# Kernel optimization log

Hardware: AMD Instinct MI355X
Metric: run time of the kernel (lower is better)

## Reference

```python
import jax, jax.numpy as jnp
import numpy as np

K_STEPS = 12      # number_of_prediction_steps
TEMP = 0.1        # temperature
EPS = 1e-12       # F.normalize eps


def setup_inputs() -> dict:
    key = jax.random.key(0)
    ks = jax.random.split(key, 8)
    B, T, W, D, C = 128, 512, 64, 128, 256
    g = lambda k, shape, s: (jax.random.normal(k, shape, jnp.float32) * s)
    return {
        "rr_windows": jax.random.normal(ks[0], (B, T, W), jnp.float32),
        # Encoder: Linear(window_size -> latent_dim)
        "We": g(ks[1], (W, D), 0.1), "be": jnp.zeros((D,), jnp.float32),
        # ARBlock: single-layer GRU(latent_dim -> context_dim)
        "Wi": g(ks[2], (D, 3 * C), 0.1), "Wh": g(ks[3], (C, 3 * C), 0.1),
        "bi": jnp.zeros((3 * C,), jnp.float32), "bh": jnp.zeros((3 * C,), jnp.float32),
        # Wk: K_STEPS Linears(context_dim -> latent_dim), stacked
        "Wk_w": g(ks[4], (K_STEPS, C, D), 0.1), "Wk_b": jnp.zeros((K_STEPS, D), jnp.float32),
    }


def _l2norm(x):
    n = jnp.linalg.norm(x, axis=-1, keepdims=True)
    return x / jnp.maximum(n, EPS)


def _gru(z_seq, Wi, Wh, bi, bh):
    # z_seq: [B, T, D] -> contexts [B, T, C]
    B = z_seq.shape[0]
    C = Wh.shape[0]
    x_proj = z_seq @ Wi + bi                       # [B, T, 3C] (precompute input gates)

    def step(h, x):
        hg = h @ Wh + bh
        xr, xz, xn = jnp.split(x, 3, axis=-1)
        hr, hz, hn = jnp.split(hg, 3, axis=-1)
        r = jax.nn.sigmoid(xr + hr)
        z = jax.nn.sigmoid(xz + hz)
        n = jnp.tanh(xn + r * hn)
        h_new = (1.0 - z) * n + z * h
        return h_new, h_new

    h0 = jnp.zeros((B, C), z_seq.dtype)
    _, hs = jax.lax.scan(step, h0, jnp.swapaxes(x_proj, 0, 1))  # [T, B, C]
    return jnp.swapaxes(hs, 0, 1)


def reference(rr_windows, We, be, Wi, Wh, bi, bh, Wk_w, Wk_b):
    B, T, W = rr_windows.shape
    # Encoder + normalize
    z_seq = _l2norm(rr_windows @ We + be)          # [B, T, D]
    # AR context
    c_seq = _gru(z_seq, Wi, Wh, bi, bh)            # [B, T, C]

    Tp = T - K_STEPS
    c_t = c_seq[:, :Tp, :]                         # [B, Tp, C]
    # all K predictions at once, then normalize
    pred = jnp.einsum('btc,kcd->kbtd', c_t, Wk_w) + Wk_b[:, None, None, :]
    pred = _l2norm(pred)                           # [K, B, Tp, D]
    # z_future[k, :, t] = z_seq[:, t + k + 1]
    zf = jnp.stack([jax.lax.dynamic_slice_in_dim(z_seq, k + 1, Tp, axis=1)
                    for k in range(K_STEPS)])      # [K, B, Tp, D]
    # logits[k, t, i, j] = pred[k, i, t] . z_future[k, j, t] / temp
    logits = jnp.einsum('kbtd,kctd->ktbc', pred, zf) / TEMP  # [K, Tp, B, B]

    lse = jax.nn.logsumexp(logits, axis=-1)        # [K, Tp, B]
    diag = jnp.einsum('ktbb->ktb', logits)
    avg_loss = jnp.mean(lse - diag)
    labels = jnp.arange(B)
    avg_accuracy = jnp.mean((jnp.argmax(logits, axis=-1) == labels).astype(jnp.float32)) * 100.0
    return avg_loss, avg_accuracy, z_seq, c_seq
```

## Files before the change

### kernel.cpp

```cpp
#include <hip/hip_runtime.h>
#include <math.h>

#define B_  128
#define T_  512
#define W_  64
#define D_  128
#define C_  256
#define K_  12
#define TP_ 500
#define N_SAMPLES 768000

typedef _Float16 half2v __attribute__((ext_vector_type(2)));
typedef _Float16 f16x8  __attribute__((ext_vector_type(8)));
typedef float    f32x4  __attribute__((ext_vector_type(4)));

__device__ __forceinline__ unsigned int pack2(float a, float b) {
  unsigned short ua = __builtin_bit_cast(unsigned short, (_Float16)a);
  unsigned short ub = __builtin_bit_cast(unsigned short, (_Float16)b);
  return (unsigned int)ua | ((unsigned int)ub << 16);
}

__global__ __launch_bounds__(128) void z_kernel(const float* __restrict__ rr,
                                                const float* __restrict__ We,
                                                const float* __restrict__ be,
                                                float* __restrict__ z_out,
                                                _Float16* __restrict__ z16) {
  int row = blockIdx.x;
  int d   = threadIdx.x;
  __shared__ float s_rr[64];
  __shared__ float s_w[2];
  if (d < 64) s_rr[d] = rr[row * 64 + d];
  __syncthreads();
  float acc = be[d];
#pragma unroll
  for (int w = 0; w < 64; ++w) acc = fmaf(s_rr[w], We[w * 128 + d], acc);
  float ss = acc * acc;
#pragma unroll
  for (int s = 1; s <= 32; s <<= 1) ss += __shfl_xor(ss, s);
  if ((d & 63) == 0) s_w[d >> 6] = ss;
  __syncthreads();
  float inv = 1.0f / fmaxf(sqrtf(s_w[0] + s_w[1]), 1e-12f);
  float zv = acc * inv;
  z_out[row * 128 + d] = zv;
  z16[(size_t)row * 128 + d] = (_Float16)zv;
}

__global__ __launch_bounds__(256) void wiT_kernel(const float* __restrict__ Wi,
                                                  _Float16* __restrict__ wiT) {
  int id = blockIdx.x * 256 + threadIdx.x;
  int k   = id / 768;
  int col = id % 768;
  wiT[(size_t)col * 128 + k] = (_Float16)Wi[id];
}

__global__ __launch_bounds__(256, 2) void xproj_mfma(const _Float16* __restrict__ z16,
                                                     const _Float16* __restrict__ wiT,
                                                     const float* __restrict__ bi,
                                                     _Float16* __restrict__ xp) {
  int rb  = blockIdx.x * 128;
  int cb  = blockIdx.y * 128;
  int tid  = threadIdx.x;
  int wv   = tid >> 6;
  int lane = tid & 63;
  int n15  = lane & 15;
  int q    = lane >> 4;

  __shared__ __align__(16) _Float16 sA[128 * 72];
  __shared__ __align__(16) _Float16 sB[128 * 72];

  f32x4 acc[2][8];
#pragma unroll
  for (int a = 0; a < 2; ++a)
#pragma unroll
    for (int m = 0; m < 8; ++m) acc[a][m] = (f32x4){0.f, 0.f, 0.f, 0.f};

#pragma unroll
  for (int p = 0; p < 2; ++p) {
#pragma unroll
    for (int it = 0; it < 4; ++it) {
      int id = tid + it * 256;
      int r  = id >> 3;
      int c8 = (id & 7) * 8;
      *(uint4*)(&sA[r * 72 + c8]) =
          *(const uint4*)(z16 + (size_t)(rb + r) * 128 + p * 64 + c8);
      *(uint4*)(&sB[r * 72 + c8]) =
          *(const uint4*)(wiT + (size_t)(cb + r) * 128 + p * 64 + c8);
    }
    __syncthreads();
#pragma unroll
    for (int ks = 0; ks < 2; ++ks) {
      f16x8 bf[2];
#pragma unroll
      for (int ntl = 0; ntl < 2; ++ntl)
        bf[ntl] = *(const f16x8*)(&sB[((wv * 2 + ntl) * 16 + n15) * 72 + ks * 32 + q * 8]);
#pragma unroll
      for (int mt = 0; mt < 8; ++mt) {
        f16x8 af = *(const f16x8*)(&sA[(mt * 16 + n15) * 72 + ks * 32 + q * 8]);
        acc[0][mt] = __builtin_amdgcn_mfma_f32_16x16x32_f16(af, bf[0], acc[0][mt], 0, 0, 0);
        acc[1][mt] = __builtin_amdgcn_mfma_f32_16x16x32_f16(af, bf[1], acc[1][mt], 0, 0, 0);
      }
    }
    __syncthreads();
  }

#pragma unroll
  for (int ntl = 0; ntl < 2; ++ntl) {
    int col = cb + (wv * 2 + ntl) * 16 + n15;
    float bb = bi[col];
#pragma unroll
    for (int mt = 0; mt < 8; ++mt) {
#pragma unroll
      for (int r = 0; r < 4; ++r) {
        int row = rb + mt * 16 + q * 4 + r;
        xp[(size_t)row * 768 + col] = (_Float16)(acc[ntl][mt][r] + bb);
      }
    }
  }
}

__global__ __launch_bounds__(256) void whT_kernel(const float* __restrict__ Wh,
                                                  unsigned int* __restrict__ whT) {
  int g = blockIdx.x * 256 + threadIdx.x;
  int i = g / 768;
  int j = g % 768;
  float lo = Wh[(size_t)(2 * i) * 768 + j];
  float hi = Wh[(size_t)(2 * i + 1) * 768 + j];
  whT[(size_t)j * 128 + i] = pack2(lo, hi);
}

__global__ __launch_bounds__(256) void wkT_kernel(const float* __restrict__ Wk_w,
                                                  _Float16* __restrict__ wkT) {
  int id = blockIdx.x * 256 + threadIdx.x;
  int k = id >> 15;
  int rem = id & 32767;
  int c = rem >> 7;
  int d = rem & 127;
  wkT[((size_t)k * 128 + d) * 256 + c] = (_Float16)Wk_w[id];
}

__global__ __launch_bounds__(1024) void gru_kernel(const _Float16* __restrict__ xp,
                                                   const unsigned int* __restrict__ whT,
                                                   const float* __restrict__ bh,
                                                   float* __restrict__ c_out,
                                                   _Float16* __restrict__ c16) {
  __shared__ __align__(16) unsigned int s_h2[2][128];
  int tid  = threadIdx.x;
  int b    = blockIdx.x;
  int w    = tid >> 6;
  int lane = tid & 63;
  int n15  = lane & 15;
  int q    = lane >> 4;
  int ch   = w * 16 + n15;

  uint4 wf[3][8];
#pragma unroll
  for (int g = 0; g < 3; ++g) {
    const uint4* src = (const uint4*)(whT + (size_t)(g * 256 + ch) * 128);
#pragma unroll
    for (int kt = 0; kt < 8; ++kt) wf[g][kt] = src[kt * 4 + q];
  }

  if (tid < 128) s_h2[0][tid] = 0u;

  float bhr = bh[ch], bhz = bh[256 + ch], bhn = bh[512 + ch];
  const _Float16* xb = xp + (size_t)b * 512 * 768;
  float xr_n = (float)xb[ch];
  float xz_n = (float)xb[256 + ch];
  float xn_n = (float)xb[512 + ch];
  float h = 0.f;
  __syncthreads();

  for (int t = 0; t < 512; ++t) {
    const char* hb = (const char*)(&s_h2[t & 1][0]) + q * 16;

    float xr_c = xr_n, xz_c = xz_n, xn_c = xn_n;
    if (t < 511) {
      const _Float16* p = xb + (size_t)(t + 1) * 768;
      xr_n = (float)p[ch];
      xz_n = (float)p[256 + ch];
      xn_n = (float)p[512 + ch];
    }

    f32x4 a0 = (f32x4){0.f, 0.f, 0.f, 0.f};
    f32x4 a1 = (f32x4){0.f, 0.f, 0.f, 0.f};
    f32x4 a2 = (f32x4){0.f, 0.f, 0.f, 0.f};
#pragma unroll
    for (int kt = 0; kt < 8; ++kt) {
      f16x8 af = *(const f16x8*)(hb + kt * 64);
      a0 = __builtin_amdgcn_mfma_f32_16x16x32_f16(af, __builtin_bit_cast(f16x8, wf[0][kt]), a0, 0, 0, 0);
      a1 = __builtin_amdgcn_mfma_f32_16x16x32_f16(af, __builtin_bit_cast(f16x8, wf[1][kt]), a1, 0, 0, 0);
      a2 = __builtin_amdgcn_mfma_f32_16x16x32_f16(af, __builtin_bit_cast(f16x8, wf[2][kt]), a2, 0, 0, 0);
    }

    float hr = a0[0] + bhr;
    float hz = a1[0] + bhz;
    float hn = a2[0] + bhn;
    float r = __builtin_amdgcn_rcpf(1.f + __expf(-(xr_c + hr)));
    float z = __builtin_amdgcn_rcpf(1.f + __expf(-(xz_c + hz)));
    float y = xn_c + r * hn;
    y = fminf(10.f, fmaxf(-10.f, y));
    float ey = __expf(-2.f * y);
    float n = (1.f - ey) * __builtin_amdgcn_rcpf(1.f + ey);
    h = (1.f - z) * n + z * h;

    if (q == 0) {
      ((_Float16*)(&s_h2[(t & 1) ^ 1][0]))[ch] = (_Float16)h;
      c_out[((size_t)b * 512 + t) * 256 + ch] = h;
      c16[((size_t)b * 512 + t) * 256 + ch] = (_Float16)h;
    }

    asm volatile("s_waitcnt lgkmcnt(0)" ::: "memory");
    __builtin_amdgcn_s_barrier();
    __builtin_amdgcn_sched_barrier(0);
  }
}

__global__ __launch_bounds__(256, 2) void cpc_kernel(const _Float16* __restrict__ z16,
                                                     const _Float16* __restrict__ c16,
                                                     const _Float16* __restrict__ wkT,
                                                     const float* __restrict__ Wk_b,
                                                     float2* __restrict__ partials) {
  int k   = blockIdx.x;
  int t   = blockIdx.y;
  int tid = threadIdx.x;
  int wv   = tid >> 6;
  int lane = tid & 63;
  int n15  = lane & 15;
  int q    = lane >> 4;

  __shared__ __align__(16) _Float16 sA[128 * 72];
  __shared__ __align__(16) _Float16 sB[128 * 72];
  __shared__ __align__(16) _Float16 sP[128 * 136];
  __shared__ float s_bias[128];

  if (tid < 128) s_bias[tid] = Wk_b[k * 128 + tid];

  f32x4 acc[2][8];
#pragma unroll
  for (int a = 0; a < 2; ++a)
#pragma unroll
    for (int m = 0; m < 8; ++m) acc[a][m] = (f32x4){0.f, 0.f, 0.f, 0.f};

  const _Float16* wk_base = wkT + (size_t)k * 128 * 256;

  for (int p = 0; p < 4; ++p) {
#pragma unroll
    for (int it = 0; it < 4; ++it) {
      int id = tid + it * 256;
      int r  = id >> 3;
      int c8 = (id & 7) * 8;
      *(uint4*)(&sA[r * 72 + c8]) =
          *(const uint4*)(wk_base + (size_t)r * 256 + p * 64 + c8);
      *(uint4*)(&sB[r * 72 + c8]) =
          *(const uint4*)(c16 + ((size_t)r * 512 + t) * 256 + p * 64 + c8);
    }
    __syncthreads();
#pragma unroll
    for (int ks = 0; ks < 2; ++ks) {
      f16x8 bf[2];
#pragma unroll
      for (int ntl = 0; ntl < 2; ++ntl)
        bf[ntl] = *(const f16x8*)(&sB[((wv * 2 + ntl) * 16 + n15) * 72 + ks * 32 + q * 8]);
#pragma unroll
      for (int mt = 0; mt < 8; ++mt) {
        f16x8 af = *(const f16x8*)(&sA[(mt * 16 + n15) * 72 + ks * 32 + q * 8]);
        acc[0][mt] = __builtin_amdgcn_mfma_f32_16x16x32_f16(af, bf[0], acc[0][mt], 0, 0, 0);
        acc[1][mt] = __builtin_amdgcn_mfma_f32_16x16x32_f16(af, bf[1], acc[1][mt], 0, 0, 0);
      }
    }
    __syncthreads();
  }

  float scale[2];
#pragma unroll
  for (int ntl = 0; ntl < 2; ++ntl) {
    float ssq = 0.f;
#pragma unroll
    for (int mt = 0; mt < 8; ++mt)
#pragma unroll
      for (int r = 0; r < 4; ++r) {
        float v = acc[ntl][mt][r] + s_bias[mt * 16 + q * 4 + r];
        acc[ntl][mt][r] = v;
        ssq = fmaf(v, v, ssq);
      }
    ssq += __shfl_xor(ssq, 16);
    ssq += __shfl_xor(ssq, 32);
    scale[ntl] = 10.0f / fmaxf(sqrtf(ssq), 1e-12f);
  }

#pragma unroll
  for (int ntl = 0; ntl < 2; ++ntl) {
    int bi = (wv * 2 + ntl) * 16 + n15;
#pragma unroll
    for (int mt = 0; mt < 8; ++mt) {
      uint2 v;
      v.x = pack2(acc[ntl][mt][0] * scale[ntl], acc[ntl][mt][1] * scale[ntl]);
      v.y = pack2(acc[ntl][mt][2] * scale[ntl], acc[ntl][mt][3] * scale[ntl]);
      *(uint2*)(&sP[bi * 136 + mt * 16 + q * 4]) = v;
    }
  }

  int tz = t + k + 1;
#pragma unroll
  for (int it = 0; it < 4; ++it) {
    int id = tid + it * 256;
    int r  = id >> 3;
    int d8 = (id & 7) * 8;
    *(uint4*)(&sA[r * 72 + d8]) =
        *(const uint4*)(z16 + ((size_t)r * 512 + tz) * 128 + d8);
    *(uint4*)(&sB[r * 72 + d8]) =
        *(const uint4*)(z16 + ((size_t)r * 512 + tz) * 128 + 64 + d8);
  }
  __syncthreads();

  f32x4 lacc[2][8];
#pragma unroll
  for (int a = 0; a < 2; ++a)
#pragma unroll
    for (int m = 0; m < 8; ++m) lacc[a][m] = (f32x4){0.f, 0.f, 0.f, 0.f};

#pragma unroll
  for (int pan = 0; pan < 2; ++pan) {
#pragma unroll
    for (int ks = 0; ks < 2; ++ks) {
      f16x8 af[2];
#pragma unroll
      for (int mtl = 0; mtl < 2; ++mtl)
        af[mtl] = *(const f16x8*)(&sP[((wv * 2 + mtl) * 16 + n15) * 136 + pan * 64 + ks * 32 + q * 8]);
#pragma unroll
      for (int nt = 0; nt < 8; ++nt) {
        f16x8 bf = pan
          ? *(const f16x8*)(&sB[(nt * 16 + n15) * 72 + ks * 32 + q * 8])
          : *(const f16x8*)(&sA[(nt * 16 + n15) * 72 + ks * 32 + q * 8]);
        lacc[0][nt] = __builtin_amdgcn_mfma_f32_16x16x32_f16(af[0], bf, lacc[0][nt], 0, 0, 0);
        lacc[1][nt] = __builtin_amdgcn_mfma_f32_16x16x32_f16(af[1], bf, lacc[1][nt], 0, 0, 0);
      }
    }
  }

  float loss_acc = 0.f, corr_acc = 0.f;
#pragma unroll
  for (int mtl = 0; mtl < 2; ++mtl) {
    int dnt = wv * 2 + mtl;
#pragma unroll
    for (int r = 0; r < 4; ++r) {
      int b = (wv * 2 + mtl) * 16 + q * 4 + r;
      float m = -1e30f; int idx = 1 << 30; float diag = 0.f;
#pragma unroll
      for (int nt = 0; nt < 8; ++nt) {
        float v = lacc[mtl][nt][r];
        int c2 = nt * 16 + n15;
        if (v > m) { m = v; idx = c2; }
        if (nt == dnt && n15 == (b & 15)) diag = v;
      }
#pragma unroll
      for (int s = 1; s <= 8; s <<= 1) {
        float om = __shfl_xor(m, s);
        int   oi = __shfl_xor(idx, s);
        if (om > m || (om == m && oi < idx)) { m = om; idx = oi; }
      }
      float e = 0.f;
#pragma unroll
      for (int nt = 0; nt < 8; ++nt) e += __expf(lacc[mtl][nt][r] - m);
#pragma unroll
      for (int s = 1; s <= 8; s <<= 1) e += __shfl_xor(e, s);
      if (n15 == (b & 15)) {
        float lse = m + __logf(e);
        loss_acc += lse - diag;
        corr_acc += (idx == b) ? 1.0f : 0.0f;
      }
    }
  }
#pragma unroll
  for (int s = 1; s <= 32; s <<= 1) {
    loss_acc += __shfl_xor(loss_acc, s);
    corr_acc += __shfl_xor(corr_acc, s);
  }

  if (lane == 0) {
    s_bias[wv * 2 + 0] = loss_acc;
    s_bias[wv * 2 + 1] = corr_acc;
  }
  __syncthreads();
  if (tid == 0) {
    float L = s_bias[0] + s_bias[2] + s_bias[4] + s_bias[6];
    float C = s_bias[1] + s_bias[3] + s_bias[5] + s_bias[7];
    partials[k * TP_ + t] = make_float2(L, C);
  }
}

__global__ __launch_bounds__(256) void reduce_kernel(const float2* __restrict__ partials,
                                                     float* __restrict__ out) {
  float l = 0.f, c = 0.f;
  for (int i = threadIdx.x; i < K_ * TP_; i += 256) {
    float2 v = partials[i];
    l += v.x; c += v.y;
  }
#pragma unroll
  for (int s = 1; s <= 32; s <<= 1) {
    l += __shfl_xor(l, s);
    c += __shfl_xor(c, s);
  }
  __shared__ float sl[4], sc[4];
  int wv = threadIdx.x >> 6;
  if ((threadIdx.x & 63) == 0) { sl[wv] = l; sc[wv] = c; }
  __syncthreads();
  if (threadIdx.x == 0) {
    float L = sl[0] + sl[1] + sl[2] + sl[3];
    float C = sc[0] + sc[1] + sc[2] + sc[3];
    out[0] = L * (float)(1.0 / (double)N_SAMPLES);
    out[1] = C * (float)(100.0 / (double)N_SAMPLES);
  }
}

extern "C" void kernel_launch(void* const* d_in, const int* in_sizes, int n_in,
                              void* d_out, int out_size, void* d_ws, size_t ws_size,
                              hipStream_t stream) {
  (void)in_sizes; (void)n_in; (void)out_size; (void)ws_size;
  const float* rr  = (const float*)d_in[0];
  const float* We  = (const float*)d_in[1];
  const float* be  = (const float*)d_in[2];
  const float* Wi  = (const float*)d_in[3];
  const float* Wh  = (const float*)d_in[4];
  const float* bi  = (const float*)d_in[5];
  const float* bh  = (const float*)d_in[6];
  const float* Wkw = (const float*)d_in[7];
  const float* Wkb = (const float*)d_in[8];

  float* out = (float*)d_out;
  float* z   = out + 2;
  float* c   = z + (size_t)B_ * T_ * D_;

  char* ws = (char*)d_ws;
  unsigned int* whT   = (unsigned int*)ws;
  _Float16*     wkT16 = (_Float16*)(ws + 393216);
  _Float16*     z16   = (_Float16*)(ws + 1179648);
  _Float16*     c16   = (_Float16*)(ws + 17956864);
  _Float16*     xp    = (_Float16*)(ws + 51511296);
  _Float16*     wiT16 = (_Float16*)(ws + 152174592);
  float2*       parts = (float2*)(ws + 51511296);

  hipMemsetAsync(d_out, 0, 2 * sizeof(float), stream);
  z_kernel<<<B_ * T_, 128, 0, stream>>>(rr, We, be, z, z16);
  wiT_kernel<<<384, 256, 0, stream>>>(Wi, wiT16);
  whT_kernel<<<384, 256, 0, stream>>>(Wh, whT);
  wkT_kernel<<<1536, 256, 0, stream>>>(Wkw, wkT16);
  xproj_mfma<<<dim3(512, 6), 256, 0, stream>>>(z16, wiT16, bi, xp);
  gru_kernel<<<B_, 1024, 0, stream>>>(xp, whT, bh, c, c16);
  cpc_kernel<<<dim3(K_, TP_), 256, 0, stream>>>(z16, c16, wkT16, Wkb, parts);
  reduce_kernel<<<1, 256, 0, stream>>>(parts, out);
}
```

Measured before the change: 982.9 us.

## Cut cpc_kernel LDS footprint and merge weight packing kernels

Three weight-transpose kernels are merged into one launch to save launch overhead. In cpc_kernel the sA tile is removed: Wk operand fragments are now read straight from global memory (where they should mostly hit cache), and the z_future tile is loaded into sB in two halves with an extra barrier. The smaller LDS footprint lets launch bounds ask for 3 blocks per CU instead of 2. The cost is uncoalesced global loads inside the MFMA loop and an extra synchronization per block.

```diff
diff --git a/kernel.cpp b/kernel.cpp
--- a/kernel.cpp
+++ b/kernel.cpp
@@ -45,12 +45,34 @@
   z16[(size_t)row * 128 + d] = (_Float16)zv;
 }
 
-__global__ __launch_bounds__(256) void wiT_kernel(const float* __restrict__ Wi,
-                                                  _Float16* __restrict__ wiT) {
-  int id = blockIdx.x * 256 + threadIdx.x;
-  int k   = id / 768;
-  int col = id % 768;
-  wiT[(size_t)col * 128 + k] = (_Float16)Wi[id];
+__global__ __launch_bounds__(256) void pack_kernel(const float* __restrict__ Wi,
+                                                   const float* __restrict__ Wh,
+                                                   const float* __restrict__ Wk_w,
+                                                   _Float16* __restrict__ wiT,
+                                                   unsigned int* __restrict__ whT,
+                                                   _Float16* __restrict__ wkT) {
+  int bid = blockIdx.x;
+  int tid = threadIdx.x;
+  if (bid < 384) {
+    int id  = bid * 256 + tid;
+    int k   = id / 768;
+    int col = id % 768;
+    wiT[(size_t)col * 128 + k] = (_Float16)Wi[id];
+  } else if (bid < 768) {
+    int g = (bid - 384) * 256 + tid;
+    int i = g / 768;
+    int j = g % 768;
+    float lo = Wh[(size_t)(2 * i) * 768 + j];
+    float hi = Wh[(size_t)(2 * i + 1) * 768 + j];
+    whT[(size_t)j * 128 + i] = pack2(lo, hi);
+  } else {
+    int id  = (bid - 768) * 256 + tid;
+    int k   = id >> 15;
+    int rem = id & 32767;
+    int c   = rem >> 7;
+    int d   = rem & 127;
+    wkT[((size_t)k * 128 + d) * 256 + c] = (_Float16)Wk_w[id];
+  }
 }
 
 __global__ __launch_bounds__(256, 2) void xproj_mfma(const _Float16* __restrict__ z16,
@@ -116,26 +138,6 @@
       }
     }
   }
-}
-
-__global__ __launch_bounds__(256) void whT_kernel(const float* __restrict__ Wh,
-                                                  unsigned int* __restrict__ whT) {
-  int g = blockIdx.x * 256 + threadIdx.x;
-  int i = g / 768;
-  int j = g % 768;
-  float lo = Wh[(size_t)(2 * i) * 768 + j];
-  float hi = Wh[(size_t)(2 * i + 1) * 768 + j];
-  whT[(size_t)j * 128 + i] = pack2(lo, hi);
-}
-
-__global__ __launch_bounds__(256) void wkT_kernel(const float* __restrict__ Wk_w,
-                                                  _Float16* __restrict__ wkT) {
-  int id = blockIdx.x * 256 + threadIdx.x;
-  int k = id >> 15;
-  int rem = id & 32767;
-  int c = rem >> 7;
-  int d = rem & 127;
-  wkT[((size_t)k * 128 + d) * 256 + c] = (_Float16)Wk_w[id];
 }
 
 __global__ __launch_bounds__(1024) void gru_kernel(const _Float16* __restrict__ xp,
@@ -215,7 +217,7 @@
   }
 }
 
-__global__ __launch_bounds__(256, 2) void cpc_kernel(const _Float16* __restrict__ z16,
+__global__ __launch_bounds__(256, 3) void cpc_kernel(const _Float16* __restrict__ z16,
                                                      const _Float16* __restrict__ c16,
                                                      const _Float16* __restrict__ wkT,
                                                      const float* __restrict__ Wk_b,
@@ -228,7 +230,6 @@
   int n15  = lane & 15;
   int q    = lane >> 4;
 
-  __shared__ __align__(16) _Float16 sA[128 * 72];
   __shared__ __align__(16) _Float16 sB[128 * 72];
   __shared__ __align__(16) _Float16 sP[128 * 136];
   __shared__ float s_bias[128];
@@ -249,8 +250,6 @@
       int id = tid + it * 256;
       int r  = id >> 3;
       int c8 = (id & 7) * 8;
-      *(uint4*)(&sA[r * 72 + c8]) =
-          *(const uint4*)(wk_base + (size_t)r * 256 + p * 64 + c8);
       *(uint4*)(&sB[r * 72 + c8]) =
           *(const uint4*)(c16 + ((size_t)r * 512 + t) * 256 + p * 64 + c8);
     }
@@ -263,7 +262,7 @@
         bf[ntl] = *(const f16x8*)(&sB[((wv * 2 + ntl) * 16 + n15) * 72 + ks * 32 + q * 8]);
 #pragma unroll
       for (int mt = 0; mt < 8; ++mt) {
-        f16x8 af = *(const f16x8*)(&sA[(mt * 16 + n15) * 72 + ks * 32 + q * 8]);
+        f16x8 af = *(const f16x8*)(wk_base + (size_t)(mt * 16 + n15) * 256 + p * 64 + ks * 32 + q * 8);
         acc[0][mt] = __builtin_amdgcn_mfma_f32_16x16x32_f16(af, bf[0], acc[0][mt], 0, 0, 0);
         acc[1][mt] = __builtin_amdgcn_mfma_f32_16x16x32_f16(af, bf[1], acc[1][mt], 0, 0, 0);
       }
@@ -301,18 +300,6 @@
   }
 
   int tz = t + k + 1;
-#pragma unroll
-  for (int it = 0; it < 4; ++it) {
-    int id = tid + it * 256;
-    int r  = id >> 3;
-    int d8 = (id & 7) * 8;
-    *(uint4*)(&sA[r * 72 + d8]) =
-        *(const uint4*)(z16 + ((size_t)r * 512 + tz) * 128 + d8);
-    *(uint4*)(&sB[r * 72 + d8]) =
-        *(const uint4*)(z16 + ((size_t)r * 512 + tz) * 128 + 64 + d8);
-  }
-  __syncthreads();
-
   f32x4 lacc[2][8];
 #pragma unroll
   for (int a = 0; a < 2; ++a)
@@ -321,6 +308,16 @@
 
 #pragma unroll
   for (int pan = 0; pan < 2; ++pan) {
+    if (pan) __syncthreads();
+#pragma unroll
+    for (int it = 0; it < 4; ++it) {
+      int id = tid + it * 256;
+      int r  = id >> 3;
+      int d8 = (id & 7) * 8;
+      *(uint4*)(&sB[r * 72 + d8]) =
+          *(const uint4*)(z16 + ((size_t)r * 512 + tz) * 128 + pan * 64 + d8);
+    }
+    __syncthreads();
 #pragma unroll
     for (int ks = 0; ks < 2; ++ks) {
       f16x8 af[2];
@@ -329,9 +326,7 @@
         af[mtl] = *(const f16x8*)(&sP[((wv * 2 + mtl) * 16 + n15) * 136 + pan * 64 + ks * 32 + q * 8]);
 #pragma unroll
       for (int nt = 0; nt < 8; ++nt) {
-        f16x8 bf = pan
-          ? *(const f16x8*)(&sB[(nt * 16 + n15) * 72 + ks * 32 + q * 8])
-          : *(const f16x8*)(&sA[(nt * 16 + n15) * 72 + ks * 32 + q * 8]);
+        f16x8 bf = *(const f16x8*)(&sB[(nt * 16 + n15) * 72 + ks * 32 + q * 8]);
         lacc[0][nt] = __builtin_amdgcn_mfma_f32_16x16x32_f16(af[0], bf, lacc[0][nt], 0, 0, 0);
         lacc[1][nt] = __builtin_amdgcn_mfma_f32_16x16x32_f16(af[1], bf, lacc[1][nt], 0, 0, 0);
       }
@@ -442,9 +437,7 @@
 
   hipMemsetAsync(d_out, 0, 2 * sizeof(float), stream);
   z_kernel<<<B_ * T_, 128, 0, stream>>>(rr, We, be, z, z16);
-  wiT_kernel<<<384, 256, 0, stream>>>(Wi, wiT16);
-  whT_kernel<<<384, 256, 0, stream>>>(Wh, whT);
-  wkT_kernel<<<1536, 256, 0, stream>>>(Wkw, wkT16);
+  pack_kernel<<<2304, 256, 0, stream>>>(Wi, Wh, Wkw, wiT16, whT, wkT16);
   xproj_mfma<<<dim3(512, 6), 256, 0, stream>>>(z16, wiT16, bi, xp);
   gru_kernel<<<B_, 1024, 0, stream>>>(xp, whT, bh, c, c16);
   cpc_kernel<<<dim3(K_, TP_), 256, 0, stream>>>(z16, c16, wkT16, Wkb, parts);
```

New measurement: 1.051 ms. 6.9% more time.
